# Optimization experiments

Hardware: AMD Instinct MI355X
Metric: run time of the kernel (lower is better)

The kernel has to match this reference:

```python
import jax, jax.numpy as jnp
import numpy as np

N, E, NFEAT, NHID = 50000, 800000, 256, 128
EPS = 1e-5


def setup_inputs() -> dict:
    key = jax.random.key(0)
    ks = jax.random.split(key, 12)
    s = 0.05
    return {
        "x": jax.random.normal(ks[0], (N, NFEAT), jnp.float32),
        "adj": jax.random.randint(ks[1], (2, E), 0, N, jnp.int32),
        "features": jax.random.uniform(ks[2], (E,), jnp.float32),
        "W_in": jax.random.normal(ks[3], (NHID, NFEAT), jnp.float32) * s,
        "b_in": jnp.zeros((NHID,), jnp.float32),
        "W1_rel": jax.random.normal(ks[4], (NHID, NHID), jnp.float32) * s,
        "b1_rel": jnp.zeros((NHID,), jnp.float32),
        "W1_root": jax.random.normal(ks[5], (NHID, NHID), jnp.float32) * s,
        "W2_rel": jax.random.normal(ks[6], (NHID, NHID), jnp.float32) * s,
        "b2_rel": jnp.zeros((NHID,), jnp.float32),
        "W2_root": jax.random.normal(ks[7], (NHID, NHID), jnp.float32) * s,
        "gamma": jnp.ones((NHID,), jnp.float32),
        "beta": jnp.zeros((NHID,), jnp.float32),
    }


def _graph_conv(h, src, dst, ew, W_rel, b_rel, W_root):
    # torch_geometric GraphConv (aggr='add'):
    #   out_i = W_rel @ (sum_{j->i} e_ji * h_j) + b_rel + W_root @ h_i
    msg = h[src] * ew[:, None]                       # [E, NHID] gather
    agg = jax.ops.segment_sum(msg, dst, num_segments=N)  # [N, NHID] scatter-add
    return agg @ W_rel.T + b_rel + h @ W_root.T


def _batch_norm(h, gamma, beta):
    mu = h.mean(axis=0)
    var = h.var(axis=0)
    return (h - mu) * jax.lax.rsqrt(var + EPS) * gamma + beta


def reference(x, adj, features, W_in, b_in, W1_rel, b1_rel, W1_root,
              W2_rel, b2_rel, W2_root, gamma, beta):
    src, dst = adj[0], adj[1]
    h = jax.nn.relu(x @ W_in.T + b_in)               # linear_in + relu (dropout=identity in eval)
    h = _graph_conv(h, src, dst, features, W1_rel, b1_rel, W1_root)
    h = jax.nn.relu(_batch_norm(h, gamma, beta))     # batch1 + relu
    h = _graph_conv(h, src, dst, features, W2_rel, b2_rel, W2_root)
    return _batch_norm(h, gamma, beta)               # batch1 reused (per source)
```

## Files before the change

### kernel.cpp

```cpp
#include <hip/hip_runtime.h>
#include <hip/hip_bf16.h>

#define NNODES 50000
#define NEDGES 800000
#define NF 256
#define NH 128
#define BN_EPS 1e-5f
#define MTILES (NNODES / 16)
#define GEMM_BLOCKS 512
#define NBUCKETS 196
#define BCAP 4608
#define SCAT_BLOCKS ((NEDGES + 2047) / 2048)

typedef __attribute__((ext_vector_type(8))) __bf16 bf16x8;
typedef __attribute__((ext_vector_type(4))) float floatx4;

__device__ __forceinline__ __hip_bfloat16 f2bf(float f) { return __float2bfloat16(f); }
__device__ __forceinline__ float bits2f(unsigned short b) {
    union { unsigned u; float f; } u; u.u = ((unsigned)b) << 16; return u.f;
}

__device__ __forceinline__ bf16x8 cvt8(const float* __restrict__ p) {
    floatx4 a0 = *(const floatx4*)p;
    floatx4 a1 = *(const floatx4*)(p + 4);
    bf16x8 r;
    r[0] = (__bf16)a0[0]; r[1] = (__bf16)a0[1]; r[2] = (__bf16)a0[2]; r[3] = (__bf16)a0[3];
    r[4] = (__bf16)a1[0]; r[5] = (__bf16)a1[1]; r[6] = (__bf16)a1[2]; r[7] = (__bf16)a1[3];
    return r;
}

__global__ __launch_bounds__(256) void convert_w_kernel(
    const float* __restrict__ W_in, const float* __restrict__ W1r,
    const float* __restrict__ W1o, const float* __restrict__ W2r,
    const float* __restrict__ W2o, __hip_bfloat16* __restrict__ wbf,
    int* __restrict__ gcursor, float* __restrict__ st1, float* __restrict__ st2)
{
    const int i = blockIdx.x * 256 + threadIdx.x;
    if (blockIdx.x == 0 && threadIdx.x < NBUCKETS)
        gcursor[threadIdx.x] = threadIdx.x * BCAP;
    if (blockIdx.x == 1) { st1[threadIdx.x] = 0.f; st2[threadIdx.x] = 0.f; }
    const float* src; int off;
    if (i < 32768)      { src = W_in; off = i; }
    else if (i < 49152) { src = W1r;  off = i - 32768; }
    else if (i < 65536) { src = W1o;  off = i - 49152; }
    else if (i < 81920) { src = W2r;  off = i - 65536; }
    else                { src = W2o;  off = i - 81920; }
    wbf[i] = f2bf(src[off]);
}

__global__ __launch_bounds__(256, 4) void scatter_gemm_in_kernel(
    const int* __restrict__ adj, const float* __restrict__ ew,
    int* __restrict__ gcursor, uint2* __restrict__ pairbuf,
    unsigned char* __restrict__ nodebuf,
    const float* __restrict__ X, const __hip_bfloat16* __restrict__ W,
    const float* __restrict__ bias, __hip_bfloat16* __restrict__ out)
{
    __shared__ int cnt[NBUCKETS];
    __shared__ int base[NBUCKETS];
    const int tid = threadIdx.x;

    if (blockIdx.x < SCAT_BLOCKS) {
        if (tid < NBUCKETS) cnt[tid] = 0;
        __syncthreads();
        const int e0 = blockIdx.x * 2048;
        #pragma unroll
        for (int i = 0; i < 8; ++i) {
            const int e = e0 + i * 256 + tid;
            if (e < NEDGES) atomicAdd(&cnt[adj[NEDGES + e] >> 8], 1);
        }
        __syncthreads();
        if (tid < NBUCKETS) {
            base[tid] = atomicAdd(&gcursor[tid], cnt[tid]);
            cnt[tid] = 0;
        }
        __syncthreads();
        #pragma unroll
        for (int i = 0; i < 8; ++i) {
            const int e = e0 + i * 256 + tid;
            if (e >= NEDGES) continue;
            const int dst = adj[NEDGES + e];
            const int b = dst >> 8;
            const int off = atomicAdd(&cnt[b], 1);
            const int slot = base[b] + off;
            if (slot < (b + 1) * BCAP) {
                pairbuf[slot] = make_uint2((unsigned)adj[e], __float_as_uint(ew[e]));
                nodebuf[slot] = (unsigned char)(dst & 255);
            }
        }
    } else {
        const int q4   = tid >> 6;
        const int lane = tid & 63;
        const int ar = lane & 15;
        const int q  = lane >> 4;

        bf16x8 bw[2][8];
        float bv[2];
        #pragma unroll
        for (int tt = 0; tt < 2; ++tt) {
            const int row = q4 * 32 + tt * 16 + ar;
            bv[tt] = bias[row];
            #pragma unroll
            for (int k = 0; k < 8; ++k)
                bw[tt][k] = *(const bf16x8*)(W + (size_t)row * NF + k * 32 + q * 8);
        }

        for (int s = blockIdx.x - SCAT_BLOCKS; s < MTILES; s += GEMM_BLOCKS) {
            const int m0 = s << 4;
            floatx4 acc[2] = {};
            #pragma unroll
            for (int k = 0; k < 8; ++k) {
                const bf16x8 a = cvt8(X + (size_t)(m0 + ar) * NF + k * 32 + q * 8);
                acc[0] = __builtin_amdgcn_mfma_f32_16x16x32_bf16(a, bw[0][k], acc[0], 0, 0, 0);
                acc[1] = __builtin_amdgcn_mfma_f32_16x16x32_bf16(a, bw[1][k], acc[1], 0, 0, 0);
            }
            #pragma unroll
            for (int tt = 0; tt < 2; ++tt) {
                const int col = q4 * 32 + tt * 16 + ar;
                #pragma unroll
                for (int r = 0; r < 4; ++r) {
                    const float v = fmaxf(acc[tt][r] + bv[tt], 0.f);
                    out[(size_t)(m0 + q * 4 + r) * NH + col] = f2bf(v);
                }
            }
        }
    }
}

__global__ __launch_bounds__(256) void bucket_sort_kernel(
    const int* __restrict__ gcursor, const uint2* __restrict__ pairbuf,
    const unsigned char* __restrict__ nodebuf, uint2* __restrict__ sorted,
    int* __restrict__ rowptr, int* __restrict__ rowend)
{
    const int b = blockIdx.x;
    const int tid = threadIdx.x;
    const int capbase = b * BCAP;
    int n = gcursor[b] - capbase;
    if (n > BCAP) n = BCAP;

    __shared__ int cnt[256];
    __shared__ int s[256];
    cnt[tid] = 0;
    __syncthreads();
    for (int j = tid; j < n; j += 256)
        atomicAdd(&cnt[nodebuf[capbase + j]], 1);
    __syncthreads();
    const int v = cnt[tid];
    s[tid] = v;
    __syncthreads();
    for (int off = 1; off < 256; off <<= 1) {
        const int t = (tid >= off) ? s[tid - off] : 0;
        __syncthreads();
        s[tid] += t;
        __syncthreads();
    }
    const int excl = s[tid] - v;
    const int node = b * 256 + tid;
    if (node < NNODES) {
        rowptr[node] = capbase + excl;
        rowend[node] = capbase + excl + v;
    }
    cnt[tid] = excl;
    __syncthreads();
    for (int j = tid; j < n; j += 256) {
        const int nd = nodebuf[capbase + j];
        const int pos = atomicAdd(&cnt[nd], 1);
        sorted[capbase + pos] = pairbuf[capbase + j];
    }
}

__global__ __launch_bounds__(256) void gather_kernel(
    const uint2* __restrict__ sorted, const int* __restrict__ rowptr,
    const int* __restrict__ rowend,
    const __hip_bfloat16* __restrict__ h, __hip_bfloat16* __restrict__ agg)
{
    const int node = blockIdx.x * 4 + (threadIdx.x >> 6);
    if (node >= NNODES) return;
    const int lane = threadIdx.x & 63;
    const int beg = rowptr[node];
    const int end = rowend[node];
    const unsigned short* hb = (const unsigned short*)h;

    float a0[8] = {}, a1[8] = {};

    int j = beg;
    if ((j & 1) && j < end) {
        const uint2 ev = sorted[j++];
        const float w = __uint_as_float(ev.y);
        const unsigned raw = *(const unsigned*)(hb + (size_t)ev.x * NH + lane * 2);
        a0[0] += w * bits2f((unsigned short)(raw & 0xffffu));
        a1[0] += w * bits2f((unsigned short)(raw >> 16));
    }
    for (; j + 8 <= end; j += 8) {
        const uint4 e01 = *(const uint4*)(sorted + j);
        const uint4 e23 = *(const uint4*)(sorted + j + 2);
        const uint4 e45 = *(const uint4*)(sorted + j + 4);
        const uint4 e67 = *(const uint4*)(sorted + j + 6);
        const unsigned r0 = *(const unsigned*)(hb + (size_t)e01.x * NH + lane * 2);
        const unsigned r1 = *(const unsigned*)(hb + (size_t)e01.z * NH + lane * 2);
        const unsigned r2 = *(const unsigned*)(hb + (size_t)e23.x * NH + lane * 2);
        const unsigned r3 = *(const unsigned*)(hb + (size_t)e23.z * NH + lane * 2);
        const unsigned r4 = *(const unsigned*)(hb + (size_t)e45.x * NH + lane * 2);
        const unsigned r5 = *(const unsigned*)(hb + (size_t)e45.z * NH + lane * 2);
        const unsigned r6 = *(const unsigned*)(hb + (size_t)e67.x * NH + lane * 2);
        const unsigned r7 = *(const unsigned*)(hb + (size_t)e67.z * NH + lane * 2);
        const float w0 = __uint_as_float(e01.y), w1 = __uint_as_float(e01.w);
        const float w2 = __uint_as_float(e23.y), w3 = __uint_as_float(e23.w);
        const float w4 = __uint_as_float(e45.y), w5 = __uint_as_float(e45.w);
        const float w6 = __uint_as_float(e67.y), w7 = __uint_as_float(e67.w);
        a0[0] += w0 * bits2f((unsigned short)(r0 & 0xffffu));
        a1[0] += w0 * bits2f((unsigned short)(r0 >> 16));
        a0[1] += w1 * bits2f((unsigned short)(r1 & 0xffffu));
        a1[1] += w1 * bits2f((unsigned short)(r1 >> 16));
        a0[2] += w2 * bits2f((unsigned short)(r2 & 0xffffu));
        a1[2] += w2 * bits2f((unsigned short)(r2 >> 16));
        a0[3] += w3 * bits2f((unsigned short)(r3 & 0xffffu));
        a1[3] += w3 * bits2f((unsigned short)(r3 >> 16));
        a0[4] += w4 * bits2f((unsigned short)(r4 & 0xffffu));
        a1[4] += w4 * bits2f((unsigned short)(r4 >> 16));
        a0[5] += w5 * bits2f((unsigned short)(r5 & 0xffffu));
        a1[5] += w5 * bits2f((unsigned short)(r5 >> 16));
        a0[6] += w6 * bits2f((unsigned short)(r6 & 0xffffu));
        a1[6] += w6 * bits2f((unsigned short)(r6 >> 16));
        a0[7] += w7 * bits2f((unsigned short)(r7 & 0xffffu));
        a1[7] += w7 * bits2f((unsigned short)(r7 >> 16));
    }
    for (; j + 2 <= end; j += 2) {
        const uint4 e01 = *(const uint4*)(sorted + j);
        const unsigned r0 = *(const unsigned*)(hb + (size_t)e01.x * NH + lane * 2);
        const unsigned r1 = *(const unsigned*)(hb + (size_t)e01.z * NH + lane * 2);
        const float w0 = __uint_as_float(e01.y), w1 = __uint_as_float(e01.w);
        a0[0] += w0 * bits2f((unsigned short)(r0 & 0xffffu));
        a1[0] += w0 * bits2f((unsigned short)(r0 >> 16));
        a0[1] += w1 * bits2f((unsigned short)(r1 & 0xffffu));
        a1[1] += w1 * bits2f((unsigned short)(r1 >> 16));
    }
    if (j < end) {
        const uint2 ev = sorted[j];
        const float w = __uint_as_float(ev.y);
        const unsigned raw = *(const unsigned*)(hb + (size_t)ev.x * NH + lane * 2);
        a0[0] += w * bits2f((unsigned short)(raw & 0xffffu));
        a1[0] += w * bits2f((unsigned short)(raw >> 16));
    }
    const float f0 = ((a0[0] + a0[1]) + (a0[2] + a0[3])) + ((a0[4] + a0[5]) + (a0[6] + a0[7]));
    const float f1 = ((a1[0] + a1[1]) + (a1[2] + a1[3])) + ((a1[4] + a1[5]) + (a1[6] + a1[7]));
    unsigned o = ((unsigned)__bfloat16_as_ushort(f2bf(f1)) << 16) |
                 (unsigned)__bfloat16_as_ushort(f2bf(f0));
    *(unsigned*)((unsigned short*)agg + (size_t)node * NH + lane * 2) = o;
}

__global__ __launch_bounds__(256, 4) void gemm_conv_kernel(
    const __hip_bfloat16* __restrict__ agg, const __hip_bfloat16* __restrict__ h,
    const __hip_bfloat16* __restrict__ Wrel, const __hip_bfloat16* __restrict__ Wroot,
    const float* __restrict__ bias, __hip_bfloat16* __restrict__ out,
    float* __restrict__ stats)
{
    const int q4   = threadIdx.x >> 6;
    const int lane = threadIdx.x & 63;
    const int ar = lane & 15;
    const int q  = lane >> 4;

    bf16x8 brel[2][4], brt[2][4];
    float bv[2];
    #pragma unroll
    for (int tt = 0; tt < 2; ++tt) {
        const int row = q4 * 32 + tt * 16 + ar;
        bv[tt] = bias[row];
        #pragma unroll
        for (int k = 0; k < 4; ++k) {
            brel[tt][k] = *(const bf16x8*)(Wrel + (size_t)row * NH + k * 32 + q * 8);
            brt[tt][k]  = *(const bf16x8*)(Wroot + (size_t)row * NH + k * 32 + q * 8);
        }
    }

    float s1[2] = {}, s2[2] = {};

    for (int s = blockIdx.x; s < MTILES; s += GEMM_BLOCKS) {
        const int m0 = s << 4;
        floatx4 acc[2] = {};
        #pragma unroll
        for (int k = 0; k < 4; ++k) {
            const bf16x8 a = *(const bf16x8*)(agg + (size_t)(m0 + ar) * NH + k * 32 + q * 8);
            acc[0] = __builtin_amdgcn_mfma_f32_16x16x32_bf16(a, brel[0][k], acc[0], 0, 0, 0);
            acc[1] = __builtin_amdgcn_mfma_f32_16x16x32_bf16(a, brel[1][k], acc[1], 0, 0, 0);
        }
        #pragma unroll
        for (int k = 0; k < 4; ++k) {
            const bf16x8 a = *(const bf16x8*)(h + (size_t)(m0 + ar) * NH + k * 32 + q * 8);
            acc[0] = __builtin_amdgcn_mfma_f32_16x16x32_bf16(a, brt[0][k], acc[0], 0, 0, 0);
            acc[1] = __builtin_amdgcn_mfma_f32_16x16x32_bf16(a, brt[1][k], acc[1], 0, 0, 0);
        }
        #pragma unroll
        for (int tt = 0; tt < 2; ++tt) {
            const int col = q4 * 32 + tt * 16 + ar;
            #pragma unroll
            for (int r = 0; r < 4; ++r) {
                const float v = acc[tt][r] + bv[tt];
                out[(size_t)(m0 + q * 4 + r) * NH + col] = f2bf(v);
                s1[tt] += v; s2[tt] += v * v;
            }
        }
    }

    __shared__ float sst[256];
    sst[threadIdx.x] = 0.f;
    __syncthreads();
    #pragma unroll
    for (int tt = 0; tt < 2; ++tt) {
        float a = s1[tt], b = s2[tt];
        a += __shfl_xor(a, 16, 64); a += __shfl_xor(a, 32, 64);
        b += __shfl_xor(b, 16, 64); b += __shfl_xor(b, 32, 64);
        if (q == 0) {
            const int col = q4 * 32 + tt * 16 + ar;
            atomicAdd(&sst[col], a);
            atomicAdd(&sst[128 + col], b);
        }
    }
    __syncthreads();
    unsafeAtomicAdd(&stats[threadIdx.x], sst[threadIdx.x]);
}

__global__ __launch_bounds__(256) void bn_relu_bf16_kernel(
    const __hip_bfloat16* __restrict__ t, const float* __restrict__ stats,
    const float* __restrict__ gamma, const float* __restrict__ beta,
    __hip_bfloat16* __restrict__ out)
{
    const size_t i = (size_t)blockIdx.x * blockDim.x + threadIdx.x;
    const int c = (int)(i & (NH - 1));
    const float inv_n = 1.0f / (float)NNODES;
    const float mu = stats[c] * inv_n;
    const float var = stats[128 + c] * inv_n - mu * mu;
    const float rs = rsqrtf(var + BN_EPS);
    float v = (__bfloat162float(t[i]) - mu) * rs * gamma[c] + beta[c];
    out[i] = f2bf(fmaxf(v, 0.f));
}

__global__ __launch_bounds__(256) void bn_f32_kernel(
    const __hip_bfloat16* __restrict__ t, const float* __restrict__ stats,
    const float* __restrict__ gamma, const float* __restrict__ beta,
    float* __restrict__ out)
{
    const size_t i = (size_t)blockIdx.x * blockDim.x + threadIdx.x;
    const int c = (int)(i & (NH - 1));
    const float inv_n = 1.0f / (float)NNODES;
    const float mu = stats[c] * inv_n;
    const float var = stats[128 + c] * inv_n - mu * mu;
    const float rs = rsqrtf(var + BN_EPS);
    out[i] = (__bfloat162float(t[i]) - mu) * rs * gamma[c] + beta[c];
}


extern "C" void kernel_launch(void* const* d_in, const int* in_sizes, int n_in,
                              void* d_out, int out_size, void* d_ws, size_t ws_size,
                              hipStream_t stream)
{
    const float* x    = (const float*)d_in[0];
    const int*   adj  = (const int*)d_in[1];
    const float* ew   = (const float*)d_in[2];
    const float* W_in = (const float*)d_in[3];
    const float* b_in = (const float*)d_in[4];
    const float* W1r  = (const float*)d_in[5];
    const float* b1   = (const float*)d_in[6];
    const float* W1o  = (const float*)d_in[7];
    const float* W2r  = (const float*)d_in[8];
    const float* b2   = (const float*)d_in[9];
    const float* W2o  = (const float*)d_in[10];
    const float* gmm  = (const float*)d_in[11];
    const float* bta  = (const float*)d_in[12];
    float* out = (float*)d_out;

    char* ws = (char*)d_ws;
    __hip_bfloat16* h0  = (__hip_bfloat16*)ws; ws += (size_t)NNODES * NH * 2;
    __hip_bfloat16* h1  = (__hip_bfloat16*)ws; ws += (size_t)NNODES * NH * 2;
    __hip_bfloat16* agg = (__hip_bfloat16*)ws; ws += (size_t)NNODES * NH * 2;
    __hip_bfloat16* t   = (__hip_bfloat16*)ws; ws += (size_t)NNODES * NH * 2;
    uint2*          sorted  = (uint2*)ws;      ws += (size_t)NBUCKETS * BCAP * 8;
    uint2*          pairbuf = (uint2*)ws;      ws += (size_t)NBUCKETS * BCAP * 8;
    unsigned char*  nodebuf = (unsigned char*)ws; ws += (size_t)NBUCKETS * BCAP;
    int*            rowptr  = (int*)ws;        ws += NNODES * 4;
    int*            rowend  = (int*)ws;        ws += NNODES * 4;
    int*            gcursor = (int*)ws;        ws += ((NBUCKETS + 3) & ~3) * 4;
    __hip_bfloat16* wbf     = (__hip_bfloat16*)ws; ws += 98304 * 2;
    float*          st1     = (float*)ws;      ws += 256 * 4;
    float*          st2     = (float*)ws;      ws += 256 * 4;

    const __hip_bfloat16* Wb_in = wbf;
    const __hip_bfloat16* Wb1r  = wbf + 32768;
    const __hip_bfloat16* Wb1o  = wbf + 49152;
    const __hip_bfloat16* Wb2r  = wbf + 65536;
    const __hip_bfloat16* Wb2o  = wbf + 81920;

    const int node_blocks = (NNODES + 3) / 4;
    const int bn_blocks   = (NNODES * NH) / 256;

    convert_w_kernel<<<98304 / 256, 256, 0, stream>>>(W_in, W1r, W1o, W2r, W2o,
                                                      wbf, gcursor, st1, st2);
    scatter_gemm_in_kernel<<<SCAT_BLOCKS + GEMM_BLOCKS, 256, 0, stream>>>(
        adj, ew, gcursor, pairbuf, nodebuf, x, Wb_in, b_in, h0);
    bucket_sort_kernel<<<NBUCKETS, 256, 0, stream>>>(gcursor, pairbuf, nodebuf,
                                                     sorted, rowptr, rowend);

    gather_kernel<<<node_blocks, 256, 0, stream>>>(sorted, rowptr, rowend, h0, agg);
    gemm_conv_kernel<<<GEMM_BLOCKS, 256, 0, stream>>>(agg, h0, Wb1r, Wb1o, b1, t, st1);
    bn_relu_bf16_kernel<<<bn_blocks, 256, 0, stream>>>(t, st1, gmm, bta, h1);

    gather_kernel<<<node_blocks, 256, 0, stream>>>(sorted, rowptr, rowend, h1, agg);
    gemm_conv_kernel<<<GEMM_BLOCKS, 256, 0, stream>>>(agg, h1, Wb2r, Wb2o, b2, t, st2);
    bn_f32_kernel<<<bn_blocks, 256, 0, stream>>>(t, st2, gmm, bta, out);
}
```

Measured before the change: 334.1 us.

## Fuse first BN+ReLU into gather and second conv GEMM, split scatter from input GEMM

Removes the standalone BN+ReLU pass over the first conv output. The affine normalisation and ReLU are now applied on the fly when gathering neighbour rows and when loading root rows in the second conv GEMM. This saves one full read and write of the hidden activations, at the cost of recomputing BN on every gathered element, which is about 16x redundant per node. It also splits the fused scatter+input-GEMM kernel into two separate launches and doubles the GEMM block count.

```diff
diff --git a/kernel.cpp b/kernel.cpp
--- a/kernel.cpp
+++ b/kernel.cpp
@@ -7,7 +7,7 @@
 #define NH 128
 #define BN_EPS 1e-5f
 #define MTILES (NNODES / 16)
-#define GEMM_BLOCKS 512
+#define GEMM_BLOCKS 1024
 #define NBUCKETS 196
 #define BCAP 4608
 #define SCAT_BLOCKS ((NEDGES + 2047) / 2048)
@@ -48,80 +48,39 @@
     wbf[i] = f2bf(src[off]);
 }
 
-__global__ __launch_bounds__(256, 4) void scatter_gemm_in_kernel(
+__global__ __launch_bounds__(256) void bucket_scatter_kernel(
     const int* __restrict__ adj, const float* __restrict__ ew,
     int* __restrict__ gcursor, uint2* __restrict__ pairbuf,
-    unsigned char* __restrict__ nodebuf,
-    const float* __restrict__ X, const __hip_bfloat16* __restrict__ W,
-    const float* __restrict__ bias, __hip_bfloat16* __restrict__ out)
+    unsigned char* __restrict__ nodebuf)
 {
     __shared__ int cnt[NBUCKETS];
     __shared__ int base[NBUCKETS];
     const int tid = threadIdx.x;
-
-    if (blockIdx.x < SCAT_BLOCKS) {
-        if (tid < NBUCKETS) cnt[tid] = 0;
-        __syncthreads();
-        const int e0 = blockIdx.x * 2048;
-        #pragma unroll
-        for (int i = 0; i < 8; ++i) {
-            const int e = e0 + i * 256 + tid;
-            if (e < NEDGES) atomicAdd(&cnt[adj[NEDGES + e] >> 8], 1);
-        }
-        __syncthreads();
-        if (tid < NBUCKETS) {
-            base[tid] = atomicAdd(&gcursor[tid], cnt[tid]);
-            cnt[tid] = 0;
-        }
-        __syncthreads();
-        #pragma unroll
-        for (int i = 0; i < 8; ++i) {
-            const int e = e0 + i * 256 + tid;
-            if (e >= NEDGES) continue;
-            const int dst = adj[NEDGES + e];
-            const int b = dst >> 8;
-            const int off = atomicAdd(&cnt[b], 1);
-            const int slot = base[b] + off;
-            if (slot < (b + 1) * BCAP) {
-                pairbuf[slot] = make_uint2((unsigned)adj[e], __float_as_uint(ew[e]));
-                nodebuf[slot] = (unsigned char)(dst & 255);
-            }
-        }
-    } else {
-        const int q4   = tid >> 6;
-        const int lane = tid & 63;
-        const int ar = lane & 15;
-        const int q  = lane >> 4;
-
-        bf16x8 bw[2][8];
-        float bv[2];
-        #pragma unroll
-        for (int tt = 0; tt < 2; ++tt) {
-            const int row = q4 * 32 + tt * 16 + ar;
-            bv[tt] = bias[row];
-            #pragma unroll
-            for (int k = 0; k < 8; ++k)
-                bw[tt][k] = *(const bf16x8*)(W + (size_t)row * NF + k * 32 + q * 8);
-        }
-
-        for (int s = blockIdx.x - SCAT_BLOCKS; s < MTILES; s += GEMM_BLOCKS) {
-            const int m0 = s << 4;
-            floatx4 acc[2] = {};
-            #pragma unroll
-            for (int k = 0; k < 8; ++k) {
-                const bf16x8 a = cvt8(X + (size_t)(m0 + ar) * NF + k * 32 + q * 8);
-                acc[0] = __builtin_amdgcn_mfma_f32_16x16x32_bf16(a, bw[0][k], acc[0], 0, 0, 0);
-                acc[1] = __builtin_amdgcn_mfma_f32_16x16x32_bf16(a, bw[1][k], acc[1], 0, 0, 0);
-            }
-            #pragma unroll
-            for (int tt = 0; tt < 2; ++tt) {
-                const int col = q4 * 32 + tt * 16 + ar;
-                #pragma unroll
-                for (int r = 0; r < 4; ++r) {
-                    const float v = fmaxf(acc[tt][r] + bv[tt], 0.f);
-                    out[(size_t)(m0 + q * 4 + r) * NH + col] = f2bf(v);
-                }
-            }
+    if (tid < NBUCKETS) cnt[tid] = 0;
+    __syncthreads();
+    const int e0 = blockIdx.x * 2048;
+    #pragma unroll
+    for (int i = 0; i < 8; ++i) {
+        const int e = e0 + i * 256 + tid;
+        if (e < NEDGES) atomicAdd(&cnt[adj[NEDGES + e] >> 8], 1);
+    }
+    __syncthreads();
+    if (tid < NBUCKETS) {
+        base[tid] = atomicAdd(&gcursor[tid], cnt[tid]);
+        cnt[tid] = 0;
+    }
+    __syncthreads();
+    #pragma unroll
+    for (int i = 0; i < 8; ++i) {
+        const int e = e0 + i * 256 + tid;
+        if (e >= NEDGES) continue;
+        const int dst = adj[NEDGES + e];
+        const int b = dst >> 8;
+        const int off = atomicAdd(&cnt[b], 1);
+        const int slot = base[b] + off;
+        if (slot < (b + 1) * BCAP) {
+            pairbuf[slot] = make_uint2((unsigned)adj[e], __float_as_uint(ew[e]));
+            nodebuf[slot] = (unsigned char)(dst & 255);
         }
     }
 }
@@ -165,6 +124,47 @@
         const int nd = nodebuf[capbase + j];
         const int pos = atomicAdd(&cnt[nd], 1);
         sorted[capbase + pos] = pairbuf[capbase + j];
+    }
+}
+
+__global__ __launch_bounds__(256, 4) void gemm_in_kernel(
+    const float* __restrict__ X, const __hip_bfloat16* __restrict__ W,
+    const float* __restrict__ bias, __hip_bfloat16* __restrict__ out)
+{
+    const int q4   = threadIdx.x >> 6;
+    const int lane = threadIdx.x & 63;
+    const int ar = lane & 15;
+    const int q  = lane >> 4;
+
+    bf16x8 bw[2][8];
+    float bv[2];
+    #pragma unroll
+    for (int tt = 0; tt < 2; ++tt) {
+        const int row = q4 * 32 + tt * 16 + ar;
+        bv[tt] = bias[row];
+        #pragma unroll
+        for (int k = 0; k < 8; ++k)
+            bw[tt][k] = *(const bf16x8*)(W + (size_t)row * NF + k * 32 + q * 8);
+    }
+
+    for (int s = blockIdx.x; s < MTILES; s += GEMM_BLOCKS) {
+        const int m0 = s << 4;
+        floatx4 acc[2] = {};
+        #pragma unroll
+        for (int k = 0; k < 8; ++k) {
+            const bf16x8 a = cvt8(X + (size_t)(m0 + ar) * NF + k * 32 + q * 8);
+            acc[0] = __builtin_amdgcn_mfma_f32_16x16x32_bf16(a, bw[0][k], acc[0], 0, 0, 0);
+            acc[1] = __builtin_amdgcn_mfma_f32_16x16x32_bf16(a, bw[1][k], acc[1], 0, 0, 0);
+        }
+        #pragma unroll
+        for (int tt = 0; tt < 2; ++tt) {
+            const int col = q4 * 32 + tt * 16 + ar;
+            #pragma unroll
+            for (int r = 0; r < 4; ++r) {
+                const float v = fmaxf(acc[tt][r] + bv[tt], 0.f);
+                out[(size_t)(m0 + q * 4 + r) * NH + col] = f2bf(v);
+            }
+        }
     }
 }
 
@@ -181,7 +181,6 @@
     const unsigned short* hb = (const unsigned short*)h;
 
     float a0[8] = {}, a1[8] = {};
-
     int j = beg;
     if ((j & 1) && j < end) {
         const uint2 ev = sorted[j++];
@@ -248,16 +247,110 @@
     *(unsigned*)((unsigned short*)agg + (size_t)node * NH + lane * 2) = o;
 }
 
+__global__ __launch_bounds__(256) void gather_bn_kernel(
+    const uint2* __restrict__ sorted, const int* __restrict__ rowptr,
+    const int* __restrict__ rowend,
+    const __hip_bfloat16* __restrict__ t1, const float* __restrict__ st,
+    const float* __restrict__ gamma, const float* __restrict__ beta,
+    __hip_bfloat16* __restrict__ agg)
+{
+    const int node = blockIdx.x * 4 + (threadIdx.x >> 6);
+    if (node >= NNODES) return;
+    const int lane = threadIdx.x & 63;
+    const int c0 = lane * 2, c1 = c0 + 1;
+    const float inv_n = 1.0f / (float)NNODES;
+    const float mu0 = st[c0] * inv_n, mu1 = st[c1] * inv_n;
+    const float A0 = rsqrtf(st[128 + c0] * inv_n - mu0 * mu0 + BN_EPS) * gamma[c0];
+    const float A1 = rsqrtf(st[128 + c1] * inv_n - mu1 * mu1 + BN_EPS) * gamma[c1];
+    const float B0 = beta[c0] - mu0 * A0;
+    const float B1 = beta[c1] - mu1 * A1;
+
+    const int beg = rowptr[node];
+    const int end = rowend[node];
+    const unsigned short* hb = (const unsigned short*)t1;
+
+    float a0[8] = {}, a1[8] = {};
+    int j = beg;
+    if ((j & 1) && j < end) {
+        const uint2 ev = sorted[j++];
+        const float w = __uint_as_float(ev.y);
+        const unsigned raw = *(const unsigned*)(hb + (size_t)ev.x * NH + lane * 2);
+        a0[0] += w * fmaxf(bits2f((unsigned short)(raw & 0xffffu)) * A0 + B0, 0.f);
+        a1[0] += w * fmaxf(bits2f((unsigned short)(raw >> 16)) * A1 + B1, 0.f);
+    }
+    for (; j + 8 <= end; j += 8) {
+        const uint4 e01 = *(const uint4*)(sorted + j);
+        const uint4 e23 = *(const uint4*)(sorted + j + 2);
+        const uint4 e45 = *(const uint4*)(sorted + j + 4);
+        const uint4 e67 = *(const uint4*)(sorted + j + 6);
+        const unsigned r0 = *(const unsigned*)(hb + (size_t)e01.x * NH + lane * 2);
+        const unsigned r1 = *(const unsigned*)(hb + (size_t)e01.z * NH + lane * 2);
+        const unsigned r2 = *(const unsigned*)(hb + (size_t)e23.x * NH + lane * 2);
+        const unsigned r3 = *(const unsigned*)(hb + (size_t)e23.z * NH + lane * 2);
+        const unsigned r4 = *(const unsigned*)(hb + (size_t)e45.x * NH + lane * 2);
+        const unsigned r5 = *(const unsigned*)(hb + (size_t)e45.z * NH + lane * 2);
+        const unsigned r6 = *(const unsigned*)(hb + (size_t)e67.x * NH + lane * 2);
+        const unsigned r7 = *(const unsigned*)(hb + (size_t)e67.z * NH + lane * 2);
+        const float w0 = __uint_as_float(e01.y), w1 = __uint_as_float(e01.w);
+        const float w2 = __uint_as_float(e23.y), w3 = __uint_as_float(e23.w);
+        const float w4 = __uint_as_float(e45.y), w5 = __uint_as_float(e45.w);
+        const float w6 = __uint_as_float(e67.y), w7 = __uint_as_float(e67.w);
+        a0[0] += w0 * fmaxf(bits2f((unsigned short)(r0 & 0xffffu)) * A0 + B0, 0.f);
+        a1[0] += w0 * fmaxf(bits2f((unsigned short)(r0 >> 16)) * A1 + B1, 0.f);
+        a0[1] += w1 * fmaxf(bits2f((unsigned short)(r1 & 0xffffu)) * A0 + B0, 0.f);
+        a1[1] += w1 * fmaxf(bits2f((unsigned short)(r1 >> 16)) * A1 + B1, 0.f);
+        a0[2] += w2 * fmaxf(bits2f((unsigned short)(r2 & 0xffffu)) * A0 + B0, 0.f);
+        a1[2] += w2 * fmaxf(bits2f((unsigned short)(r2 >> 16)) * A1 + B1, 0.f);
+        a0[3] += w3 * fmaxf(bits2f((unsigned short)(r3 & 0xffffu)) * A0 + B0, 0.f);
+        a1[3] += w3 * fmaxf(bits2f((unsigned short)(r3 >> 16)) * A1 + B1, 0.f);
+        a0[4] += w4 * fmaxf(bits2f((unsigned short)(r4 & 0xffffu)) * A0 + B0, 0.f);
+        a1[4] += w4 * fmaxf(bits2f((unsigned short)(r4 >> 16)) * A1 + B1, 0.f);
+        a0[5] += w5 * fmaxf(bits2f((unsigned short)(r5 & 0xffffu)) * A0 + B0, 0.f);
+        a1[5] += w5 * fmaxf(bits2f((unsigned short)(r5 >> 16)) * A1 + B1, 0.f);
+        a0[6] += w6 * fmaxf(bits2f((unsigned short)(r6 & 0xffffu)) * A0 + B0, 0.f);
+        a1[6] += w6 * fmaxf(bits2f((unsigned short)(r6 >> 16)) * A1 + B1, 0.f);
+        a0[7] += w7 * fmaxf(bits2f((unsigned short)(r7 & 0xffffu)) * A0 + B0, 0.f);
+        a1[7] += w7 * fmaxf(bits2f((unsigned short)(r7 >> 16)) * A1 + B1, 0.f);
+    }
+    for (; j < end; ++j) {
+        const uint2 ev = sorted[j];
+        const float w = __uint_as_float(ev.y);
+        const unsigned raw = *(const unsigned*)(hb + (size_t)ev.x * NH + lane * 2);
+        a0[0] += w * fmaxf(bits2f((unsigned short)(raw & 0xffffu)) * A0 + B0, 0.f);
+        a1[0] += w * fmaxf(bits2f((unsigned short)(raw >> 16)) * A1 + B1, 0.f);
+    }
+    const float f0 = ((a0[0] + a0[1]) + (a0[2] + a0[3])) + ((a0[4] + a0[5]) + (a0[6] + a0[7]));
+    const float f1 = ((a1[0] + a1[1]) + (a1[2] + a1[3])) + ((a1[4] + a1[5]) + (a1[6] + a1[7]));
+    unsigned o = ((unsigned)__bfloat16_as_ushort(f2bf(f1)) << 16) |
+                 (unsigned)__bfloat16_as_ushort(f2bf(f0));
+    *(unsigned*)((unsigned short*)agg + (size_t)node * NH + lane * 2) = o;
+}
+
+template <bool BN_A2>
 __global__ __launch_bounds__(256, 4) void gemm_conv_kernel(
-    const __hip_bfloat16* __restrict__ agg, const __hip_bfloat16* __restrict__ h,
+    const __hip_bfloat16* __restrict__ agg, const __hip_bfloat16* __restrict__ hsrc,
     const __hip_bfloat16* __restrict__ Wrel, const __hip_bfloat16* __restrict__ Wroot,
-    const float* __restrict__ bias, __hip_bfloat16* __restrict__ out,
-    float* __restrict__ stats)
+    const float* __restrict__ bias, const float* __restrict__ bnstats,
+    const float* __restrict__ gamma, const float* __restrict__ beta,
+    __hip_bfloat16* __restrict__ out, float* __restrict__ stats)
 {
     const int q4   = threadIdx.x >> 6;
     const int lane = threadIdx.x & 63;
     const int ar = lane & 15;
     const int q  = lane >> 4;
+
+    __shared__ float sA[128], sB[128];
+    if constexpr (BN_A2) {
+        if (threadIdx.x < 128) {
+            const int c = threadIdx.x;
+            const float inv_n = 1.0f / (float)NNODES;
+            const float mu = bnstats[c] * inv_n;
+            const float a = rsqrtf(bnstats[128 + c] * inv_n - mu * mu + BN_EPS) * gamma[c];
+            sA[c] = a;
+            sB[c] = beta[c] - mu * a;
+        }
+        __syncthreads();
+    }
 
     bf16x8 brel[2][4], brt[2][4];
     float bv[2];
@@ -285,7 +378,14 @@
         }
         #pragma unroll
         for (int k = 0; k < 4; ++k) {
-            const bf16x8 a = *(const bf16x8*)(h + (size_t)(m0 + ar) * NH + k * 32 + q * 8);
+            bf16x8 a = *(const bf16x8*)(hsrc + (size_t)(m0 + ar) * NH + k * 32 + q * 8);
+            if constexpr (BN_A2) {
+                #pragma unroll
+                for (int i = 0; i < 8; ++i) {
+                    const int c = k * 32 + q * 8 + i;
+                    a[i] = (__bf16)fmaxf((float)a[i] * sA[c] + sB[c], 0.f);
+                }
+            }
             acc[0] = __builtin_amdgcn_mfma_f32_16x16x32_bf16(a, brt[0][k], acc[0], 0, 0, 0);
             acc[1] = __builtin_amdgcn_mfma_f32_16x16x32_bf16(a, brt[1][k], acc[1], 0, 0, 0);
         }
@@ -317,21 +417,6 @@
     }
     __syncthreads();
     unsafeAtomicAdd(&stats[threadIdx.x], sst[threadIdx.x]);
-}
-
-__global__ __launch_bounds__(256) void bn_relu_bf16_kernel(
-    const __hip_bfloat16* __restrict__ t, const float* __restrict__ stats,
-    const float* __restrict__ gamma, const float* __restrict__ beta,
-    __hip_bfloat16* __restrict__ out)
-{
-    const size_t i = (size_t)blockIdx.x * blockDim.x + threadIdx.x;
-    const int c = (int)(i & (NH - 1));
-    const float inv_n = 1.0f / (float)NNODES;
-    const float mu = stats[c] * inv_n;
-    const float var = stats[128 + c] * inv_n - mu * mu;
-    const float rs = rsqrtf(var + BN_EPS);
-    float v = (__bfloat162float(t[i]) - mu) * rs * gamma[c] + beta[c];
-    out[i] = f2bf(fmaxf(v, 0.f));
 }
 
 __global__ __launch_bounds__(256) void bn_f32_kernel(
@@ -370,9 +455,9 @@
 
     char* ws = (char*)d_ws;
     __hip_bfloat16* h0  = (__hip_bfloat16*)ws; ws += (size_t)NNODES * NH * 2;
-    __hip_bfloat16* h1  = (__hip_bfloat16*)ws; ws += (size_t)NNODES * NH * 2;
+    __hip_bfloat16* t1  = (__hip_bfloat16*)ws; ws += (size_t)NNODES * NH * 2;
+    __hip_bfloat16* t2  = (__hip_bfloat16*)ws; ws += (size_t)NNODES * NH * 2;
     __hip_bfloat16* agg = (__hip_bfloat16*)ws; ws += (size_t)NNODES * NH * 2;
-    __hip_bfloat16* t   = (__hip_bfloat16*)ws; ws += (size_t)NNODES * NH * 2;
     uint2*          sorted  = (uint2*)ws;      ws += (size_t)NBUCKETS * BCAP * 8;
     uint2*          pairbuf = (uint2*)ws;      ws += (size_t)NBUCKETS * BCAP * 8;
     unsigned char*  nodebuf = (unsigned char*)ws; ws += (size_t)NBUCKETS * BCAP;
@@ -394,16 +479,18 @@
 
     convert_w_kernel<<<98304 / 256, 256, 0, stream>>>(W_in, W1r, W1o, W2r, W2o,
                                                       wbf, gcursor, st1, st2);
-    scatter_gemm_in_kernel<<<SCAT_BLOCKS + GEMM_BLOCKS, 256, 0, stream>>>(
-        adj, ew, gcursor, pairbuf, nodebuf, x, Wb_in, b_in, h0);
+    gemm_in_kernel<<<GEMM_BLOCKS, 256, 0, stream>>>(x, Wb_in, b_in, h0);
+    bucket_scatter_kernel<<<SCAT_BLOCKS, 256, 0, stream>>>(adj, ew, gcursor, pairbuf, nodebuf);
     bucket_sort_kernel<<<NBUCKETS, 256, 0, stream>>>(gcursor, pairbuf, nodebuf,
                                                      sorted, rowptr, rowend);
 
     gather_kernel<<<node_blocks, 256, 0, stream>>>(sorted, rowptr, rowend, h0, agg);
-    gemm_conv_kernel<<<GEMM_BLOCKS, 256, 0, stream>>>(agg, h0, Wb1r, Wb1o, b1, t, st1);
-    bn_relu_bf16_kernel<<<bn_blocks, 256, 0, stream>>>(t, st1, gmm, bta, h1);
-
-    gather_kernel<<<node_blocks, 256, 0, stream>>>(sorted, rowptr, rowend, h1, agg);
-    gemm_conv_kernel<<<GEMM_BLOCKS, 256, 0, stream>>>(agg, h1, Wb2r, Wb2o, b2, t, st2);
-    bn_f32_kernel<<<bn_blocks, 256, 0, stream>>>(t, st2, gmm, bta, out);
-}
+    gemm_conv_kernel<false><<<GEMM_BLOCKS, 256, 0, stream>>>(
+        agg, h0, Wb1r, Wb1o, b1, nullptr, nullptr, nullptr, t1, st1);
+
+    gather_bn_kernel<<<node_blocks, 256, 0, stream>>>(sorted, rowptr, rowend,
+                                                      t1, st1, gmm, bta, agg);
+    gemm_conv_kernel<true><<<GEMM_BLOCKS, 256, 0, stream>>>(
+        agg, t1, Wb2r, Wb2o, b2, st1, gmm, bta, t2, st2);
+    bn_f32_kernel<<<bn_blocks, 256, 0, stream>>>(t2, st2, gmm, bta, out);
+}
```

Result: slower. 394.1 us (+18.0%).
